# Kernel optimization log

Hardware: AMD Instinct MI355X
Metric: run time of the kernel (lower is better)

The kernel has to match this reference:

```python
import jax, jax.numpy as jnp
import numpy as np

B, N, M, D = 2, 256, 8, 256      # batch, seq, modalities, dmodel
H, DH = 8, 64                     # heads, dim_head (hardcoded defaults)
INNER = H * DH                    # 512
MULT = 4                          # FFN mult
SCALE = DH ** -0.5
EPS = 1e-5


def layer_norm(x, g, b):
    mu = jnp.mean(x, axis=-1, keepdims=True)
    var = jnp.mean((x - mu) ** 2, axis=-1, keepdims=True)
    return (x - mu) * jax.lax.rsqrt(var + EPS) * g + b


def setup_inputs() -> dict:
    key = jax.random.key(0)
    ks = jax.random.split(key, 8)
    s = 0.02
    return {
        "x": jax.random.normal(ks[0], (B, D, M, N), jnp.float32),
        "Wq": jax.random.normal(ks[1], (D, INNER), jnp.float32) * s,
        "Wkv": jax.random.normal(ks[2], (D, 2 * INNER), jnp.float32) * s,
        "Wout": jax.random.normal(ks[3], (INNER * M, D * M), jnp.float32) * s,
        "bout": jnp.zeros((D * M,), jnp.float32),
        "g1": jnp.ones((D,), jnp.float32),
        "beta1": jnp.zeros((D,), jnp.float32),
        "Wff1": jax.random.normal(ks[4], (D, 2 * D * MULT), jnp.float32) * s,
        "bff1": jnp.zeros((2 * D * MULT,), jnp.float32),
        "Wff2": jax.random.normal(ks[5], (D * MULT, D), jnp.float32) * s,
        "bff2": jnp.zeros((D,), jnp.float32),
        "g2": jnp.ones((D,), jnp.float32),
        "beta2": jnp.zeros((D,), jnp.float32),
    }


def reference(x, Wq, Wkv, Wout, bout, g1, beta1, Wff1, bff1, Wff2, bff2, g2, beta2):
    x_shape = x.shape
    xt = jnp.transpose(x, (0, 3, 2, 1))          # [B,N,M,D]
    # --- Channel_Seq_Big_Attention (self-attention, context = x) ---
    q = (xt @ Wq).reshape(B, N, M, H, DH)
    kv = xt @ Wkv
    k, v = jnp.split(kv, 2, axis=-1)
    k = k.reshape(B, N, M, H, DH)
    v = v.reshape(B, N, M, H, DH)
    # sim: [(b h), i, j, m, z] kept as [B,H,i,j,m,z]
    sim = jnp.einsum('bimhd,bjzhd->bhijmz', q, k) * SCALE
    attn = jax.nn.softmax(sim, axis=2)           # softmax over j (dim=-3 of bijmz)
    out = jnp.einsum('bhijmz,bjmhd->bizhd', attn, v)  # [B,N,M,H,DH]
    out = out.reshape(B, N, M * H * DH)          # 'b n (m h d)'
    o = (out @ Wout + bout).reshape(B, N, M, D)
    # --- residual + post-norm ---
    xt = layer_norm(xt + o, g1, beta1)
    # --- GEGLU FFN ---
    hg = xt @ Wff1 + bff1
    a, gate = jnp.split(hg, 2, axis=-1)
    ff = (a * jax.nn.gelu(gate, approximate=False)) @ Wff2 + bff2
    xt = layer_norm(xt + ff, g2, beta2)
    return xt.reshape(x_shape)                   # torch .view(x_shape)
```

## Files before the change

kernel.cpp:

```cpp
#include <hip/hip_runtime.h>
#include <math.h>

#define KS_ 0.1803368801111244f

typedef __attribute__((ext_vector_type(8))) short bf16x8;
typedef __attribute__((ext_vector_type(4))) short bf16x4;
typedef __attribute__((ext_vector_type(4))) float f32x4;

__device__ inline short f2bf(float f) {
  unsigned u = __builtin_bit_cast(unsigned, f);
  u += 0x7fff + ((u >> 16) & 1);
  return (short)(u >> 16);
}

__device__ inline void gload16(const short* g, short* l) {
  __builtin_amdgcn_global_load_lds(
      (const __attribute__((address_space(1))) void*)g,
      (__attribute__((address_space(3))) void*)l, 16, 0, 0);
}

__device__ inline void wt_tile(const float* __restrict__ W, short* __restrict__ WT,
                               int K, int N, int bx, int by, int t, float (*tile)[33]) {
  int n0 = bx * 32, k0 = by * 32;
  int tx = t & 31, ty = t >> 5;
#pragma unroll
  for (int r = 0; r < 32; r += 8)
    tile[ty + r][tx] = W[(size_t)(k0 + ty + r) * N + n0 + tx];
  __syncthreads();
#pragma unroll
  for (int r = 0; r < 32; r += 8)
    WT[(size_t)(n0 + ty + r) * K + k0 + tx] = f2bf(tile[tx][ty + r]);
}

__global__ __launch_bounds__(256) void k_prep_all(const float* __restrict__ x, float* __restrict__ xt,
                                                  short* __restrict__ xtbf,
                                                  const float* __restrict__ Wq, const float* __restrict__ Wkv,
                                                  const float* __restrict__ Wout, const float* __restrict__ Wff1,
                                                  const float* __restrict__ Wff2,
                                                  short* __restrict__ WqkvT, short* __restrict__ WoutT,
                                                  short* __restrict__ Wff1T, short* __restrict__ Wff2T) {
  __shared__ float tile[32][33];
  int bid = blockIdx.x, t = threadIdx.x;
  if (bid < 8192) {
    wt_tile(Wout, WoutT, 4096, 2048, bid & 63, bid >> 6, t, tile);
  } else if (bid < 9216) {
    int r = bid - 8192;
    int bx = r & 7, by = (r >> 3) & 7, bm = r >> 6;
    int b = bm >> 3, m = bm & 7;
    int d0 = bx * 32, n0 = by * 32;
    int tx = t & 31, ty = t >> 5;
#pragma unroll
    for (int rr = 0; rr < 32; rr += 8) {
      int d = d0 + ty + rr, n = n0 + tx;
      tile[ty + rr][tx] = x[((size_t)(b * 256 + d) * 8 + m) * 256 + n];
    }
    __syncthreads();
#pragma unroll
    for (int rr = 0; rr < 32; rr += 8) {
      int n = n0 + ty + rr, d = d0 + tx;
      float v = tile[tx][ty + rr];
      size_t idx = ((size_t)(b * 256 + n) * 8 + m) * 256 + d;
      xt[idx] = v;
      xtbf[idx] = f2bf(v);
    }
  } else if (bid < 9344) {
    int r = bid - 9216;
    wt_tile(Wq, WqkvT, 256, 512, r & 15, r >> 4, t, tile);
  } else if (bid < 9600) {
    int r = bid - 9344;
    wt_tile(Wkv, WqkvT + 131072, 256, 1024, r & 31, r >> 5, t, tile);
  } else if (bid < 10112) {
    int r = bid - 9600;
    wt_tile(Wff1, Wff1T, 256, 2048, r & 63, r >> 6, t, tile);
  } else {
    int r = bid - 10112;
    wt_tile(Wff2, Wff2T, 1024, 256, r & 7, r >> 3, t, tile);
  }
}

__global__ __launch_bounds__(256) void k_gemm_qkv(const short* __restrict__ A, const short* __restrict__ Bt,
                                                  short* __restrict__ qfrag, short* __restrict__ kfrag,
                                                  short* __restrict__ vfrag) {
  __shared__ short As[2][2048];
  __shared__ short Bs[2][2048];
  __shared__ short Cs[64 * 72];
  int t = threadIdx.x;
  int bx = blockIdx.x, by = blockIdx.y;
  int sel = bx >> 3, h = bx & 7;
  int row0 = by * 64, col0 = bx * 64;
  int b = by >> 5, n0 = (by * 8) & 255;
  int bh = b * 8 + h;
  int w = t >> 6, lane = t & 63, quad = lane >> 4, l16 = lane & 15;
  int wr = w >> 1, wc = w & 1;
  int r = t >> 2;
  int cs = ((t & 3) ^ ((r >> 1) & 3)) * 8;
  const short* Ag = A + (size_t)(row0 + r) * 256 + cs;
  const short* Bg = Bt + (size_t)(col0 + r) * 256 + cs;
  int sw = (l16 >> 1) & 3;
  int chk = (quad ^ sw) * 8;
  int aoff[2], boff[2];
#pragma unroll
  for (int rf = 0; rf < 2; rf++) {
    aoff[rf] = (wr * 32 + rf * 16 + l16) * 32 + chk;
    boff[rf] = (wc * 32 + rf * 16 + l16) * 32 + chk;
  }
  f32x4 acc[2][2] = {{{0,0,0,0},{0,0,0,0}},{{0,0,0,0},{0,0,0,0}}};
  gload16(Ag, &As[0][w * 512]);
  gload16(Bg, &Bs[0][w * 512]);
  __syncthreads();
  int buf = 0;
  for (int k0 = 0; k0 < 256; k0 += 32) {
    int nb = buf ^ 1;
    if (k0 + 32 < 256) {
      gload16(Ag + k0 + 32, &As[nb][w * 512]);
      gload16(Bg + k0 + 32, &Bs[nb][w * 512]);
    }
    bf16x8 af[2], bf[2];
#pragma unroll
    for (int rf = 0; rf < 2; rf++) af[rf] = *(const bf16x8*)&As[buf][aoff[rf]];
#pragma unroll
    for (int cf = 0; cf < 2; cf++) bf[cf] = *(const bf16x8*)&Bs[buf][boff[cf]];
#pragma unroll
    for (int rf = 0; rf < 2; rf++)
#pragma unroll
      for (int cf = 0; cf < 2; cf++)
        acc[rf][cf] = __builtin_amdgcn_mfma_f32_16x16x32_bf16(af[rf], bf[cf], acc[rf][cf], 0, 0, 0);
    __syncthreads();
    buf = nb;
  }
  if (sel < 2) {
#pragma unroll
    for (int rf = 0; rf < 2; rf++)
#pragma unroll
      for (int cf = 0; cf < 2; cf++) {
        int col = wc * 32 + cf * 16 + l16;
#pragma unroll
        for (int rr = 0; rr < 4; rr++)
          Cs[(wr * 32 + rf * 16 + quad * 4 + rr) * 72 + col] = f2bf(acc[rf][cf][rr]);
      }
  } else {
#pragma unroll
    for (int rf = 0; rf < 2; rf++)
#pragma unroll
      for (int cf = 0; cf < 2; cf++) {
        int col = wc * 32 + cf * 16 + l16;
        bf16x4 pk;
#pragma unroll
        for (int rr = 0; rr < 4; rr++) pk[rr] = f2bf(acc[rf][cf][rr]);
        *(bf16x4*)&Cs[col * 72 + wr * 32 + rf * 16 + quad * 4] = pk;
      }
  }
  __syncthreads();
  if (sel < 2) {
    short* dst = sel ? kfrag : qfrag;
    int it = n0 >> 4, l16b = n0 & 8;
#pragma unroll
    for (int cidx = 0; cidx < 2; cidx++) {
      int chunk = t + cidx * 256;
      int m = chunk >> 6, ks2 = (chunk >> 5) & 1, q2 = (chunk >> 3) & 3, n = chunk & 7;
      bf16x8 val = *(const bf16x8*)&Cs[(n * 8 + m) * 72 + ks2 * 32 + q2 * 8];
      size_t off = ((size_t)(bh * 128 + m * 16 + it) * 2 + ks2) * 512 + (q2 * 16 + l16b + n) * 8;
      *(bf16x8*)(dst + off) = val;
    }
  } else {
    int jc = n0 >> 5, jf = (n0 >> 4) & 1, qbase = (n0 & 8) >> 2;
#pragma unroll
    for (int cidx = 0; cidx < 2; cidx++) {
      int chunk = t + cidx * 256;
      int qd = chunk >> 8, m0 = (chunk >> 6) & 3, dtt = (chunk >> 4) & 3, l16c = chunk & 15;
      int d = dtt * 16 + l16c;
      unsigned u[4];
#pragma unroll
      for (int e3 = 0; e3 < 4; e3++)
        u[e3] = *(const unsigned*)&Cs[d * 72 + qd * 32 + e3 * 8 + 2 * m0];
      uint4 pv;
      pv.x = __builtin_amdgcn_perm(u[1], u[0], 0x05040100u);
      pv.y = __builtin_amdgcn_perm(u[3], u[2], 0x05040100u);
      pv.z = __builtin_amdgcn_perm(u[1], u[0], 0x07060302u);
      pv.w = __builtin_amdgcn_perm(u[3], u[2], 0x07060302u);
      int quad2 = qbase + qd;
      size_t cid = (((size_t)(bh * 8 + jc) * 4 + m0) * 4 + dtt) * 2 + jf;
      *(bf16x8*)(vfrag + cid * 512 + (quad2 * 16 + l16c) * 8) = __builtin_bit_cast(bf16x8, pv);
    }
  }
}

__global__ __launch_bounds__(256) void k_gemm128(const short* __restrict__ A, const short* __restrict__ Bt,
                                                 const float* __restrict__ bias, float* __restrict__ C,
                                                 int M, int N, int K, int Ks) {
  __shared__ short As[2][4096];
  __shared__ short Bs[2][4096];
  int t = threadIdx.x;
  int row0 = blockIdx.y * 128, col0 = blockIdx.x * 128;
  int kp = blockIdx.z;
  int kbeg = kp * Ks, kend = kbeg + Ks;
  int w = t >> 6, lane = t & 63, quad = lane >> 4, l16 = lane & 15;
  int wr = w >> 1, wc = w & 1;
  int rs = t >> 2;
  int cs = ((t & 3) ^ ((rs >> 1) & 3)) * 8;
  const short* Ag = A + (size_t)(row0 + rs) * K + cs;
  const short* Bg = Bt + (size_t)(col0 + rs) * K + cs;
  size_t rskip = (size_t)64 * K;
  int chk = (quad ^ ((l16 >> 1) & 3)) * 8;
  int aoff[4], boff[4];
#pragma unroll
  for (int f = 0; f < 4; f++) {
    aoff[f] = (wr * 64 + f * 16 + l16) * 32 + chk;
    boff[f] = (wc * 64 + f * 16 + l16) * 32 + chk;
  }
  f32x4 acc[4][4];
#pragma unroll
  for (int i = 0; i < 4; i++)
#pragma unroll
    for (int j = 0; j < 4; j++) acc[i][j] = (f32x4){0, 0, 0, 0};
  int ld0 = w * 512;
  gload16(Ag + kbeg, &As[0][ld0]);
  gload16(Ag + rskip + kbeg, &As[0][2048 + ld0]);
  gload16(Bg + kbeg, &Bs[0][ld0]);
  gload16(Bg + rskip + kbeg, &Bs[0][2048 + ld0]);
  __syncthreads();
  int buf = 0;
  for (int k0 = kbeg; k0 < kend; k0 += 32) {
    int nb = buf ^ 1;
    if (k0 + 32 < kend) {
      gload16(Ag + k0 + 32, &As[nb][ld0]);
      gload16(Ag + rskip + k0 + 32, &As[nb][2048 + ld0]);
      gload16(Bg + k0 + 32, &Bs[nb][ld0]);
      gload16(Bg + rskip + k0 + 32, &Bs[nb][2048 + ld0]);
    }
    bf16x8 af[4], bf[4];
#pragma unroll
    for (int f = 0; f < 4; f++) af[f] = *(const bf16x8*)&As[buf][aoff[f]];
#pragma unroll
    for (int f = 0; f < 4; f++) bf[f] = *(const bf16x8*)&Bs[buf][boff[f]];
#pragma unroll
    for (int i = 0; i < 4; i++)
#pragma unroll
      for (int j = 0; j < 4; j++)
        acc[i][j] = __builtin_amdgcn_mfma_f32_16x16x32_bf16(af[i], bf[j], acc[i][j], 0, 0, 0);
    __syncthreads();
    buf = nb;
  }
  float* Cp = C + (size_t)kp * M * N;
  bool dob = (bias && kp == 0);
#pragma unroll
  for (int i = 0; i < 4; i++)
#pragma unroll
    for (int j = 0; j < 4; j++) {
      int col = col0 + wc * 64 + j * 16 + l16;
      float vb = dob ? bias[col] : 0.0f;
#pragma unroll
      for (int rr = 0; rr < 4; rr++) {
        int row = row0 + wr * 64 + i * 16 + quad * 4 + rr;
        Cp[(size_t)row * N + col] = acc[i][j][rr] + vb;
      }
    }
}

__global__ __launch_bounds__(256) void k_gemm_bf(const short* __restrict__ A, const short* __restrict__ Bt,
                                                 const float* __restrict__ bias, float* __restrict__ C,
                                                 int M, int N, int K, int Ks) {
  __shared__ short As[2][2048];
  __shared__ short Bs[2][2048];
  int t = threadIdx.x;
  int row0 = blockIdx.y * 64, col0 = blockIdx.x * 64;
  int kp = blockIdx.z;
  int kbeg = kp * Ks, kend = kbeg + Ks;
  int w = t >> 6, lane = t & 63, quad = lane >> 4, l16 = lane & 15;
  int wr = w >> 1, wc = w & 1;
  int r = t >> 2;
  int cs = ((t & 3) ^ ((r >> 1) & 3)) * 8;
  const short* Ag = A + (size_t)(row0 + r) * K + cs;
  const short* Bg = Bt + (size_t)(col0 + r) * K + cs;
  int sw = (l16 >> 1) & 3;
  int chk = (quad ^ sw) * 8;
  int aoff[2], boff[2];
#pragma unroll
  for (int rf = 0; rf < 2; rf++) {
    aoff[rf] = (wr * 32 + rf * 16 + l16) * 32 + chk;
    boff[rf] = (wc * 32 + rf * 16 + l16) * 32 + chk;
  }
  f32x4 acc[2][2] = {{{0,0,0,0},{0,0,0,0}},{{0,0,0,0},{0,0,0,0}}};
  gload16(Ag + kbeg, &As[0][w * 512]);
  gload16(Bg + kbeg, &Bs[0][w * 512]);
  __syncthreads();
  int buf = 0;
  for (int k0 = kbeg; k0 < kend; k0 += 32) {
    int nb = buf ^ 1;
    if (k0 + 32 < kend) {
      gload16(Ag + k0 + 32, &As[nb][w * 512]);
      gload16(Bg + k0 + 32, &Bs[nb][w * 512]);
    }
    bf16x8 af[2], bf[2];
#pragma unroll
    for (int rf = 0; rf < 2; rf++) af[rf] = *(const bf16x8*)&As[buf][aoff[rf]];
#pragma unroll
    for (int cf = 0; cf < 2; cf++) bf[cf] = *(const bf16x8*)&Bs[buf][boff[cf]];
#pragma unroll
    for (int rf = 0; rf < 2; rf++)
#pragma unroll
      for (int cf = 0; cf < 2; cf++)
        acc[rf][cf] = __builtin_amdgcn_mfma_f32_16x16x32_bf16(af[rf], bf[cf], acc[rf][cf], 0, 0, 0);
    __syncthreads();
    buf = nb;
  }
  float* Cp = C + (size_t)kp * M * N;
#pragma unroll
  for (int rf = 0; rf < 2; rf++)
#pragma unroll
    for (int cf = 0; cf < 2; cf++) {
      int col = col0 + wc * 32 + cf * 16 + l16;
      float vb = (bias && kp == 0) ? bias[col] : 0.0f;
#pragma unroll
      for (int rr = 0; rr < 4; rr++) {
        int row = row0 + wr * 32 + rf * 16 + quad * 4 + rr;
        Cp[(size_t)row * N + col] = acc[rf][cf][rr] + vb;
      }
    }
}

__global__ __launch_bounds__(256) void k_ff1g128(const short* __restrict__ A, const short* __restrict__ Bt,
                                                 const float* __restrict__ bias, short* __restrict__ gg) {
  __shared__ short As[2][4096];
  __shared__ short Ba[2][2048];
  __shared__ short Bg[2][2048];
  int t = threadIdx.x;
  int colA0 = blockIdx.x * 64, row0 = blockIdx.y * 128;
  int w = t >> 6, lane = t & 63, quad = lane >> 4, l16 = lane & 15;
  int wr = w >> 1, wc = w & 1;
  int rs = t >> 2;
  int cs = ((t & 3) ^ ((rs >> 1) & 3)) * 8;
  const short* Ag  = A + (size_t)(row0 + rs) * 256 + cs;
  const short* BaG = Bt + (size_t)(colA0 + rs) * 256 + cs;
  const short* BgG = Bt + (size_t)(1024 + colA0 + rs) * 256 + cs;
  int chk = (quad ^ ((l16 >> 1) & 3)) * 8;
  int aoff[4], boff[2];
#pragma unroll
  for (int f = 0; f < 4; f++) aoff[f] = (wr * 64 + f * 16 + l16) * 32 + chk;
#pragma unroll
  for (int f = 0; f < 2; f++) boff[f] = (wc * 32 + f * 16 + l16) * 32 + chk;
  f32x4 za = {0, 0, 0, 0};
  f32x4 acc_a[4][2] = {{za, za}, {za, za}, {za, za}, {za, za}};
  f32x4 acc_g[4][2] = {{za, za}, {za, za}, {za, za}, {za, za}};
  int ld0 = w * 512;
  gload16(Ag, &As[0][ld0]);
  gload16(Ag + (size_t)64 * 256, &As[0][2048 + ld0]);
  gload16(BaG, &Ba[0][ld0]);
  gload16(BgG, &Bg[0][ld0]);
  __syncthreads();
  int buf = 0;
  for (int k0 = 0; k0 < 256; k0 += 32) {
    int nb = buf ^ 1;
    if (k0 + 32 < 256) {
      gload16(Ag + k0 + 32, &As[nb][ld0]);
      gload16(Ag + (size_t)64 * 256 + k0 + 32, &As[nb][2048 + ld0]);
      gload16(BaG + k0 + 32, &Ba[nb][ld0]);
      gload16(BgG + k0 + 32, &Bg[nb][ld0]);
    }
    bf16x8 af[4], ba[2], bg[2];
#pragma unroll
    for (int f = 0; f < 4; f++) af[f] = *(const bf16x8*)&As[buf][aoff[f]];
#pragma unroll
    for (int f = 0; f < 2; f++) {
      ba[f] = *(const bf16x8*)&Ba[buf][boff[f]];
      bg[f] = *(const bf16x8*)&Bg[buf][boff[f]];
    }
#pragma unroll
    for (int i = 0; i < 4; i++)
#pragma unroll
      for (int j = 0; j < 2; j++) {
        acc_a[i][j] = __builtin_amdgcn_mfma_f32_16x16x32_bf16(af[i], ba[j], acc_a[i][j], 0, 0, 0);
        acc_g[i][j] = __builtin_amdgcn_mfma_f32_16x16x32_bf16(af[i], bg[j], acc_g[i][j], 0, 0, 0);
      }
    __syncthreads();
    buf = nb;
  }
#pragma unroll
  for (int i = 0; i < 4; i++)
#pragma unroll
    for (int j = 0; j < 2; j++) {
      int col = colA0 + wc * 32 + j * 16 + l16;
      float ba_ = bias[col], bg_ = bias[1024 + col];
#pragma unroll
      for (int rr = 0; rr < 4; rr++) {
        int row = row0 + wr * 64 + i * 16 + quad * 4 + rr;
        float a = acc_a[i][j][rr] + ba_;
        float g = acc_g[i][j][rr] + bg_;
        float ge = 0.5f * g * (1.0f + erff(g * 0.70710678118654752f));
        gg[(size_t)row * 1024 + col] = f2bf(a * ge);
      }
    }
}

__global__ __launch_bounds__(256) void k_attn_den5(const short* __restrict__ qfrag, const short* __restrict__ kfrag,
                                                   float* __restrict__ rdg) {
  int ct2 = blockIdx.x, mp = blockIdx.y, bh = blockIdx.z;
  int t = threadIdx.x;
  int w = t >> 6, lane = t & 63;
  int rt0 = ct2 * 8 + w * 2;
  bf16x8 bfr[2][2];
#pragma unroll
  for (int cf = 0; cf < 2; cf++)
#pragma unroll
    for (int ks = 0; ks < 2; ks++)
      bfr[cf][ks] = *(const bf16x8*)(kfrag + ((size_t)((bh * 128 + rt0 + cf) * 2 + ks)) * 512 + lane * 8);
  for (int mi = 0; mi < 2; mi++) {
    int m = mp * 2 + mi;
    float fa0 = 0.0f, fa1 = 0.0f;
#pragma unroll 4
    for (int it2 = 0; it2 < 16; it2++) {
      const short* ap = qfrag + ((size_t)((bh * 128 + m * 16 + it2) * 2)) * 512 + lane * 8;
      bf16x8 a0 = *(const bf16x8*)ap;
      bf16x8 a1 = *(const bf16x8*)(ap + 512);
      f32x4 c0 = {0, 0, 0, 0}, c1 = {0, 0, 0, 0};
      c0 = __builtin_amdgcn_mfma_f32_16x16x32_bf16(a0, bfr[0][0], c0, 0, 0, 0);
      c0 = __builtin_amdgcn_mfma_f32_16x16x32_bf16(a1, bfr[0][1], c0, 0, 0, 0);
      c1 = __builtin_amdgcn_mfma_f32_16x16x32_bf16(a0, bfr[1][0], c1, 0, 0, 0);
      c1 = __builtin_amdgcn_mfma_f32_16x16x32_bf16(a1, bfr[1][1], c1, 0, 0, 0);
#pragma unroll
      for (int rr = 0; rr < 4; rr++) {
        fa0 += __builtin_amdgcn_exp2f(c0[rr] * KS_);
        fa1 += __builtin_amdgcn_exp2f(c1[rr] * KS_);
      }
    }
    fa0 += __shfl_xor(fa0, 16); fa0 += __shfl_xor(fa0, 32);
    fa1 += __shfl_xor(fa1, 16); fa1 += __shfl_xor(fa1, 32);
    if (lane < 16) {
      rdg[(size_t)(bh * 8 + m) * 2048 + rt0 * 16 + lane] = -__builtin_amdgcn_logf(fa0);
      rdg[(size_t)(bh * 8 + m) * 2048 + (rt0 + 1) * 16 + lane] = -__builtin_amdgcn_logf(fa1);
    }
  }
}

__global__ __launch_bounds__(256) void k_attn_out6(const short* __restrict__ qfrag, const short* __restrict__ kfrag,
                                                   const short* __restrict__ vfrag, const float* __restrict__ rdg,
                                                   short* __restrict__ ao) {
  __shared__ float red[4 * 64 * 17];
  int z = blockIdx.x, itp = blockIdx.y, bh = blockIdx.z;
  int b = bh >> 3, h = bh & 7;
  int t = threadIdx.x, w = t >> 6, lane = t & 63, quad = lane >> 4, l16 = lane & 15;
  const float* rb = rdg + (size_t)bh * 16384;
  f32x4 z4 = {0, 0, 0, 0};
  bf16x8 qf[2][2][2];
#pragma unroll
  for (int iti = 0; iti < 2; iti++)
#pragma unroll
    for (int mm = 0; mm < 2; mm++)
#pragma unroll
      for (int ks = 0; ks < 2; ks++)
        qf[iti][mm][ks] = *(const bf16x8*)(qfrag +
            ((size_t)((bh * 128 + (2 * w + mm) * 16 + itp * 2 + iti) * 2 + ks)) * 512 + lane * 8);
  f32x4 acc[2][4];
#pragma unroll
  for (int iti = 0; iti < 2; iti++)
#pragma unroll
    for (int dt = 0; dt < 4; dt++) acc[iti][dt] = z4;
  bf16x8 vf[4][2], kf[2][2];
  float4 nv0[2], nv1[2];
#pragma unroll
  for (int dt = 0; dt < 4; dt++)
#pragma unroll
    for (int jf = 0; jf < 2; jf++)
      vf[dt][jf] = *(const bf16x8*)(vfrag + ((((size_t)(bh * 8 + 0) * 4 + w) * 4 + dt) * 2 + jf) * 512 + lane * 8);
#pragma unroll
  for (int jf = 0; jf < 2; jf++) {
    const short* kp = kfrag + ((size_t)((bh * 128 + z * 16 + 0 * 2 + jf) * 2)) * 512 + lane * 8;
    kf[jf][0] = *(const bf16x8*)kp;
    kf[jf][1] = *(const bf16x8*)(kp + 512);
    nv0[jf] = *(const float4*)(rb + (size_t)(2 * w) * 2048 + z * 256 + 0 * 32 + jf * 16 + quad * 4);
    nv1[jf] = *(const float4*)(rb + (size_t)(2 * w + 1) * 2048 + z * 256 + 0 * 32 + jf * 16 + quad * 4);
  }
  for (int jc = 0; jc < 8; jc++) {
    bf16x8 vfn[4][2], kfn[2][2];
    float4 nv0n[2], nv1n[2];
    if (jc < 7) {
      int jn = jc + 1;
#pragma unroll
      for (int dt = 0; dt < 4; dt++)
#pragma unroll
        for (int jf = 0; jf < 2; jf++)
          vfn[dt][jf] = *(const bf16x8*)(vfrag + ((((size_t)(bh * 8 + jn) * 4 + w) * 4 + dt) * 2 + jf) * 512 + lane * 8);
#pragma unroll
      for (int jf = 0; jf < 2; jf++) {
        const short* kp = kfrag + ((size_t)((bh * 128 + z * 16 + jn * 2 + jf) * 2)) * 512 + lane * 8;
        kfn[jf][0] = *(const bf16x8*)kp;
        kfn[jf][1] = *(const bf16x8*)(kp + 512);
        nv0n[jf] = *(const float4*)(rb + (size_t)(2 * w) * 2048 + z * 256 + jn * 32 + jf * 16 + quad * 4);
        nv1n[jf] = *(const float4*)(rb + (size_t)(2 * w + 1) * 2048 + z * 256 + jn * 32 + jf * 16 + quad * 4);
      }
    }
    float n0[2][4] = {{nv0[0].x, nv0[0].y, nv0[0].z, nv0[0].w}, {nv0[1].x, nv0[1].y, nv0[1].z, nv0[1].w}};
    float n1[2][4] = {{nv1[0].x, nv1[0].y, nv1[0].z, nv1[0].w}, {nv1[1].x, nv1[1].y, nv1[1].z, nv1[1].w}};
#pragma unroll
    for (int iti = 0; iti < 2; iti++) {
      f32x4 c[2][2] = {{z4, z4}, {z4, z4}};
#pragma unroll
      for (int jf = 0; jf < 2; jf++)
#pragma unroll
        for (int mm = 0; mm < 2; mm++) {
          c[jf][mm] = __builtin_amdgcn_mfma_f32_16x16x32_bf16(kf[jf][0], qf[iti][mm][0], c[jf][mm], 0, 0, 0);
          c[jf][mm] = __builtin_amdgcn_mfma_f32_16x16x32_bf16(kf[jf][1], qf[iti][mm][1], c[jf][mm], 0, 0, 0);
        }
      bf16x8 pf[2];
#pragma unroll
      for (int jf = 0; jf < 2; jf++) {
        unsigned u[8];
#pragma unroll
        for (int e = 0; e < 4; e++) {
          u[e]     = __builtin_bit_cast(unsigned, __builtin_amdgcn_exp2f(fmaf(c[jf][0][e], KS_, n0[jf][e]))) + 0x8000u;
          u[e + 4] = __builtin_bit_cast(unsigned, __builtin_amdgcn_exp2f(fmaf(c[jf][1][e], KS_, n1[jf][e]))) + 0x8000u;
        }
        uint4 pv;
        pv.x = __builtin_amdgcn_perm(u[1], u[0], 0x07060302u);
        pv.y = __builtin_amdgcn_perm(u[3], u[2], 0x07060302u);
        pv.z = __builtin_amdgcn_perm(u[5], u[4], 0x07060302u);
        pv.w = __builtin_amdgcn_perm(u[7], u[6], 0x07060302u);
        pf[jf] = __builtin_bit_cast(bf16x8, pv);
      }
#pragma unroll
      for (int dt = 0; dt < 4; dt++)
#pragma unroll
        for (int jf = 0; jf < 2; jf++)
          acc[iti][dt] = __builtin_amdgcn_mfma_f32_16x16x32_bf16(vf[dt][jf], pf[jf], acc[iti][dt], 0, 0, 0);
    }
    if (jc < 7) {
#pragma unroll
      for (int dt = 0; dt < 4; dt++)
#pragma unroll
        for (int jf = 0; jf < 2; jf++) vf[dt][jf] = vfn[dt][jf];
#pragma unroll
      for (int jf = 0; jf < 2; jf++) {
        kf[jf][0] = kfn[jf][0]; kf[jf][1] = kfn[jf][1];
        nv0[jf] = nv0n[jf]; nv1[jf] = nv1n[jf];
      }
    }
  }
  for (int iti = 0; iti < 2; iti++) {
#pragma unroll
    for (int dt = 0; dt < 4; dt++)
#pragma unroll
      for (int rr = 0; rr < 4; rr++)
        red[w * 1088 + (dt * 16 + quad * 4 + rr) * 17 + l16] = acc[iti][dt][rr];
    __syncthreads();
    {
      int i = t >> 4, dg = t & 15;
      float s[4] = {0, 0, 0, 0};
#pragma unroll
      for (int w2 = 0; w2 < 4; w2++)
#pragma unroll
        for (int r2 = 0; r2 < 4; r2++)
          s[r2] += red[w2 * 1088 + (dg * 4 + r2) * 17 + i];
      bf16x4 ov;
#pragma unroll
      for (int r2 = 0; r2 < 4; r2++) ov[r2] = f2bf(s[r2]);
      *(bf16x4*)(ao + (size_t)((b * 256 + itp * 32 + iti * 16 + i) * 8 + z) * 512 + h * 64 + dg * 4) = ov;
    }
    __syncthreads();
  }
}

__global__ __launch_bounds__(256) void k_ln(const float* __restrict__ X, const float* __restrict__ P, int np,
                                            const float* __restrict__ g, const float* __restrict__ be,
                                            float* __restrict__ Y, short* __restrict__ Ybf) {
  __shared__ float sm[8];
  int row = blockIdx.x, t = threadIdx.x;
  int lane = t & 63, w = t >> 6;
  size_t base = (size_t)row * 256;
  float v = X[base + t];
  for (int p = 0; p < np; p++) v += P[(size_t)p * 1048576 + base + t];
  float s = v;
  s += __shfl_xor(s, 1); s += __shfl_xor(s, 2); s += __shfl_xor(s, 4);
  s += __shfl_xor(s, 8); s += __shfl_xor(s, 16); s += __shfl_xor(s, 32);
  if (lane == 0) sm[w] = s;
  __syncthreads();
  float mu = (sm[0] + sm[1] + sm[2] + sm[3]) * (1.0f / 256.0f);
  float dv = v - mu;
  float s2 = dv * dv;
  s2 += __shfl_xor(s2, 1); s2 += __shfl_xor(s2, 2); s2 += __shfl_xor(s2, 4);
  s2 += __shfl_xor(s2, 8); s2 += __shfl_xor(s2, 16); s2 += __shfl_xor(s2, 32);
  if (lane == 0) sm[4 + w] = s2;
  __syncthreads();
  float var = (sm[4] + sm[5] + sm[6] + sm[7]) * (1.0f / 256.0f);
  float rs = rsqrtf(var + 1e-5f);
  float res = dv * rs * g[t] + be[t];
  Y[base + t] = res;
  if (Ybf) Ybf[base + t] = f2bf(res);
}

extern "C" void kernel_launch(void* const* d_in, const int* in_sizes, int n_in,
                              void* d_out, int out_size, void* d_ws, size_t ws_size,
                              hipStream_t stream) {
  const float* x    = (const float*)d_in[0];
  const float* Wq   = (const float*)d_in[1];
  const float* Wkv  = (const float*)d_in[2];
  const float* Wout = (const float*)d_in[3];
  const float* bout = (const float*)d_in[4];
  const float* g1   = (const float*)d_in[5];
  const float* be1  = (const float*)d_in[6];
  const float* Wff1 = (const float*)d_in[7];
  const float* bff1 = (const float*)d_in[8];
  const float* Wff2 = (const float*)d_in[9];
  const float* bff2 = (const float*)d_in[10];
  const float* g2   = (const float*)d_in[11];
  const float* be2  = (const float*)d_in[12];
  float* out = (float*)d_out;
  float* w = (float*)d_ws;

  float* xt   = w;
  float* part = w + 1048576;
  float* y    = w + 9437184;
  float* rdg  = w + 11534336;
  short* sb     = (short*)(w + 11796480);
  short* qfrag  = sb;
  short* kfrag  = sb + 2097152;
  short* vfrag  = sb + 4194304;
  short* xt_bf  = sb + 6291456;
  short* ao_bf  = sb + 7340032;
  short* y_bf   = sb + 9437184;
  short* gg_bf  = sb + 10485760;
  short* WqkvT  = sb + 14680064;
  short* WoutT  = sb + 15073280;
  short* Wff1T  = sb + 23461888;
  short* Wff2T  = sb + 23986176;

  k_prep_all<<<10368, 256, 0, stream>>>(x, xt, xt_bf, Wq, Wkv, Wout, Wff1, Wff2,
                                        WqkvT, WoutT, Wff1T, Wff2T);
  k_gemm_qkv<<<dim3(24, 64), 256, 0, stream>>>(xt_bf, WqkvT, qfrag, kfrag, vfrag);
  k_attn_den5<<<dim3(16, 4, 16), 256, 0, stream>>>(qfrag, kfrag, rdg);
  k_attn_out6<<<dim3(8, 8, 16), 256, 0, stream>>>(qfrag, kfrag, vfrag, rdg, ao_bf);
  k_gemm128<<<dim3(16, 4, 8), 256, 0, stream>>>(ao_bf, WoutT, bout, part, 512, 2048, 4096, 512);
  k_ln<<<4096, 256, 0, stream>>>(xt, part, 8, g1, be1, y, y_bf);
  k_ff1g128<<<dim3(16, 32), 256, 0, stream>>>(y_bf, Wff1T, bff1, gg_bf);
  k_gemm_bf<<<dim3(4, 64, 4), 256, 0, stream>>>(gg_bf, Wff2T, bff2, part, 4096, 256, 1024, 256);
  k_ln<<<4096, 256, 0, stream>>>(y, part, 4, g2, be2, out, nullptr);
}
```

Measured before the change: 220.8 us.

## Fuse output projection, layernorms and FFN into one cooperative persistent kernel

Replaces five separate launches (out-projection GEMM, LN1, GEGLU FF1, FF2 GEMM, LN2) with a single cooperative kernel of 256 blocks of 512 threads. Each block runs two 256-thread sub-tiles and the stages are separated by grid-wide syncs. FF2 now uses 2 K-splits instead of 4, and each LN sub-tile handles 8 rows. The aim is to remove per-launch overhead and tail gaps between stages. The cost is grid.sync barriers, fixed occupancy of one block per CU, and less parallelism in the LN and FF2 stages.

```diff
diff --git a/kernel.cpp b/kernel.cpp
--- a/kernel.cpp
+++ b/kernel.cpp
@@ -1,5 +1,8 @@
 #include <hip/hip_runtime.h>
+#include <hip/hip_cooperative_groups.h>
 #include <math.h>
+
+namespace cg = cooperative_groups;
 
 #define KS_ 0.1803368801111244f
 
@@ -185,213 +188,6 @@
   }
 }
 
-__global__ __launch_bounds__(256) void k_gemm128(const short* __restrict__ A, const short* __restrict__ Bt,
-                                                 const float* __restrict__ bias, float* __restrict__ C,
-                                                 int M, int N, int K, int Ks) {
-  __shared__ short As[2][4096];
-  __shared__ short Bs[2][4096];
-  int t = threadIdx.x;
-  int row0 = blockIdx.y * 128, col0 = blockIdx.x * 128;
-  int kp = blockIdx.z;
-  int kbeg = kp * Ks, kend = kbeg + Ks;
-  int w = t >> 6, lane = t & 63, quad = lane >> 4, l16 = lane & 15;
-  int wr = w >> 1, wc = w & 1;
-  int rs = t >> 2;
-  int cs = ((t & 3) ^ ((rs >> 1) & 3)) * 8;
-  const short* Ag = A + (size_t)(row0 + rs) * K + cs;
-  const short* Bg = Bt + (size_t)(col0 + rs) * K + cs;
-  size_t rskip = (size_t)64 * K;
-  int chk = (quad ^ ((l16 >> 1) & 3)) * 8;
-  int aoff[4], boff[4];
-#pragma unroll
-  for (int f = 0; f < 4; f++) {
-    aoff[f] = (wr * 64 + f * 16 + l16) * 32 + chk;
-    boff[f] = (wc * 64 + f * 16 + l16) * 32 + chk;
-  }
-  f32x4 acc[4][4];
-#pragma unroll
-  for (int i = 0; i < 4; i++)
-#pragma unroll
-    for (int j = 0; j < 4; j++) acc[i][j] = (f32x4){0, 0, 0, 0};
-  int ld0 = w * 512;
-  gload16(Ag + kbeg, &As[0][ld0]);
-  gload16(Ag + rskip + kbeg, &As[0][2048 + ld0]);
-  gload16(Bg + kbeg, &Bs[0][ld0]);
-  gload16(Bg + rskip + kbeg, &Bs[0][2048 + ld0]);
-  __syncthreads();
-  int buf = 0;
-  for (int k0 = kbeg; k0 < kend; k0 += 32) {
-    int nb = buf ^ 1;
-    if (k0 + 32 < kend) {
-      gload16(Ag + k0 + 32, &As[nb][ld0]);
-      gload16(Ag + rskip + k0 + 32, &As[nb][2048 + ld0]);
-      gload16(Bg + k0 + 32, &Bs[nb][ld0]);
-      gload16(Bg + rskip + k0 + 32, &Bs[nb][2048 + ld0]);
-    }
-    bf16x8 af[4], bf[4];
-#pragma unroll
-    for (int f = 0; f < 4; f++) af[f] = *(const bf16x8*)&As[buf][aoff[f]];
-#pragma unroll
-    for (int f = 0; f < 4; f++) bf[f] = *(const bf16x8*)&Bs[buf][boff[f]];
-#pragma unroll
-    for (int i = 0; i < 4; i++)
-#pragma unroll
-      for (int j = 0; j < 4; j++)
-        acc[i][j] = __builtin_amdgcn_mfma_f32_16x16x32_bf16(af[i], bf[j], acc[i][j], 0, 0, 0);
-    __syncthreads();
-    buf = nb;
-  }
-  float* Cp = C + (size_t)kp * M * N;
-  bool dob = (bias && kp == 0);
-#pragma unroll
-  for (int i = 0; i < 4; i++)
-#pragma unroll
-    for (int j = 0; j < 4; j++) {
-      int col = col0 + wc * 64 + j * 16 + l16;
-      float vb = dob ? bias[col] : 0.0f;
-#pragma unroll
-      for (int rr = 0; rr < 4; rr++) {
-        int row = row0 + wr * 64 + i * 16 + quad * 4 + rr;
-        Cp[(size_t)row * N + col] = acc[i][j][rr] + vb;
-      }
-    }
-}
-
-__global__ __launch_bounds__(256) void k_gemm_bf(const short* __restrict__ A, const short* __restrict__ Bt,
-                                                 const float* __restrict__ bias, float* __restrict__ C,
-                                                 int M, int N, int K, int Ks) {
-  __shared__ short As[2][2048];
-  __shared__ short Bs[2][2048];
-  int t = threadIdx.x;
-  int row0 = blockIdx.y * 64, col0 = blockIdx.x * 64;
-  int kp = blockIdx.z;
-  int kbeg = kp * Ks, kend = kbeg + Ks;
-  int w = t >> 6, lane = t & 63, quad = lane >> 4, l16 = lane & 15;
-  int wr = w >> 1, wc = w & 1;
-  int r = t >> 2;
-  int cs = ((t & 3) ^ ((r >> 1) & 3)) * 8;
-  const short* Ag = A + (size_t)(row0 + r) * K + cs;
-  const short* Bg = Bt + (size_t)(col0 + r) * K + cs;
-  int sw = (l16 >> 1) & 3;
-  int chk = (quad ^ sw) * 8;
-  int aoff[2], boff[2];
-#pragma unroll
-  for (int rf = 0; rf < 2; rf++) {
-    aoff[rf] = (wr * 32 + rf * 16 + l16) * 32 + chk;
-    boff[rf] = (wc * 32 + rf * 16 + l16) * 32 + chk;
-  }
-  f32x4 acc[2][2] = {{{0,0,0,0},{0,0,0,0}},{{0,0,0,0},{0,0,0,0}}};
-  gload16(Ag + kbeg, &As[0][w * 512]);
-  gload16(Bg + kbeg, &Bs[0][w * 512]);
-  __syncthreads();
-  int buf = 0;
-  for (int k0 = kbeg; k0 < kend; k0 += 32) {
-    int nb = buf ^ 1;
-    if (k0 + 32 < kend) {
-      gload16(Ag + k0 + 32, &As[nb][w * 512]);
-      gload16(Bg + k0 + 32, &Bs[nb][w * 512]);
-    }
-    bf16x8 af[2], bf[2];
-#pragma unroll
-    for (int rf = 0; rf < 2; rf++) af[rf] = *(const bf16x8*)&As[buf][aoff[rf]];
-#pragma unroll
-    for (int cf = 0; cf < 2; cf++) bf[cf] = *(const bf16x8*)&Bs[buf][boff[cf]];
-#pragma unroll
-    for (int rf = 0; rf < 2; rf++)
-#pragma unroll
-      for (int cf = 0; cf < 2; cf++)
-        acc[rf][cf] = __builtin_amdgcn_mfma_f32_16x16x32_bf16(af[rf], bf[cf], acc[rf][cf], 0, 0, 0);
-    __syncthreads();
-    buf = nb;
-  }
-  float* Cp = C + (size_t)kp * M * N;
-#pragma unroll
-  for (int rf = 0; rf < 2; rf++)
-#pragma unroll
-    for (int cf = 0; cf < 2; cf++) {
-      int col = col0 + wc * 32 + cf * 16 + l16;
-      float vb = (bias && kp == 0) ? bias[col] : 0.0f;
-#pragma unroll
-      for (int rr = 0; rr < 4; rr++) {
-        int row = row0 + wr * 32 + rf * 16 + quad * 4 + rr;
-        Cp[(size_t)row * N + col] = acc[rf][cf][rr] + vb;
-      }
-    }
-}
-
-__global__ __launch_bounds__(256) void k_ff1g128(const short* __restrict__ A, const short* __restrict__ Bt,
-                                                 const float* __restrict__ bias, short* __restrict__ gg) {
-  __shared__ short As[2][4096];
-  __shared__ short Ba[2][2048];
-  __shared__ short Bg[2][2048];
-  int t = threadIdx.x;
-  int colA0 = blockIdx.x * 64, row0 = blockIdx.y * 128;
-  int w = t >> 6, lane = t & 63, quad = lane >> 4, l16 = lane & 15;
-  int wr = w >> 1, wc = w & 1;
-  int rs = t >> 2;
-  int cs = ((t & 3) ^ ((rs >> 1) & 3)) * 8;
-  const short* Ag  = A + (size_t)(row0 + rs) * 256 + cs;
-  const short* BaG = Bt + (size_t)(colA0 + rs) * 256 + cs;
-  const short* BgG = Bt + (size_t)(1024 + colA0 + rs) * 256 + cs;
-  int chk = (quad ^ ((l16 >> 1) & 3)) * 8;
-  int aoff[4], boff[2];
-#pragma unroll
-  for (int f = 0; f < 4; f++) aoff[f] = (wr * 64 + f * 16 + l16) * 32 + chk;
-#pragma unroll
-  for (int f = 0; f < 2; f++) boff[f] = (wc * 32 + f * 16 + l16) * 32 + chk;
-  f32x4 za = {0, 0, 0, 0};
-  f32x4 acc_a[4][2] = {{za, za}, {za, za}, {za, za}, {za, za}};
-  f32x4 acc_g[4][2] = {{za, za}, {za, za}, {za, za}, {za, za}};
-  int ld0 = w * 512;
-  gload16(Ag, &As[0][ld0]);
-  gload16(Ag + (size_t)64 * 256, &As[0][2048 + ld0]);
-  gload16(BaG, &Ba[0][ld0]);
-  gload16(BgG, &Bg[0][ld0]);
-  __syncthreads();
-  int buf = 0;
-  for (int k0 = 0; k0 < 256; k0 += 32) {
-    int nb = buf ^ 1;
-    if (k0 + 32 < 256) {
-      gload16(Ag + k0 + 32, &As[nb][ld0]);
-      gload16(Ag + (size_t)64 * 256 + k0 + 32, &As[nb][2048 + ld0]);
-      gload16(BaG + k0 + 32, &Ba[nb][ld0]);
-      gload16(BgG + k0 + 32, &Bg[nb][ld0]);
-    }
-    bf16x8 af[4], ba[2], bg[2];
-#pragma unroll
-    for (int f = 0; f < 4; f++) af[f] = *(const bf16x8*)&As[buf][aoff[f]];
-#pragma unroll
-    for (int f = 0; f < 2; f++) {
-      ba[f] = *(const bf16x8*)&Ba[buf][boff[f]];
-      bg[f] = *(const bf16x8*)&Bg[buf][boff[f]];
-    }
-#pragma unroll
-    for (int i = 0; i < 4; i++)
-#pragma unroll
-      for (int j = 0; j < 2; j++) {
-        acc_a[i][j] = __builtin_amdgcn_mfma_f32_16x16x32_bf16(af[i], ba[j], acc_a[i][j], 0, 0, 0);
-        acc_g[i][j] = __builtin_amdgcn_mfma_f32_16x16x32_bf16(af[i], bg[j], acc_g[i][j], 0, 0, 0);
-      }
-    __syncthreads();
-    buf = nb;
-  }
-#pragma unroll
-  for (int i = 0; i < 4; i++)
-#pragma unroll
-    for (int j = 0; j < 2; j++) {
-      int col = colA0 + wc * 32 + j * 16 + l16;
-      float ba_ = bias[col], bg_ = bias[1024 + col];
-#pragma unroll
-      for (int rr = 0; rr < 4; rr++) {
-        int row = row0 + wr * 64 + i * 16 + quad * 4 + rr;
-        float a = acc_a[i][j][rr] + ba_;
-        float g = acc_g[i][j][rr] + bg_;
-        float ge = 0.5f * g * (1.0f + erff(g * 0.70710678118654752f));
-        gg[(size_t)row * 1024 + col] = f2bf(a * ge);
-      }
-    }
-}
-
 __global__ __launch_bounds__(256) void k_attn_den5(const short* __restrict__ qfrag, const short* __restrict__ kfrag,
                                                    float* __restrict__ rdg) {
   int ct2 = blockIdx.x, mp = blockIdx.y, bh = blockIdx.z;
@@ -559,32 +355,271 @@
   }
 }
 
-__global__ __launch_bounds__(256) void k_ln(const float* __restrict__ X, const float* __restrict__ P, int np,
-                                            const float* __restrict__ g, const float* __restrict__ be,
-                                            float* __restrict__ Y, short* __restrict__ Ybf) {
-  __shared__ float sm[8];
-  int row = blockIdx.x, t = threadIdx.x;
-  int lane = t & 63, w = t >> 6;
-  size_t base = (size_t)row * 256;
-  float v = X[base + t];
-  for (int p = 0; p < np; p++) v += P[(size_t)p * 1048576 + base + t];
-  float s = v;
-  s += __shfl_xor(s, 1); s += __shfl_xor(s, 2); s += __shfl_xor(s, 4);
-  s += __shfl_xor(s, 8); s += __shfl_xor(s, 16); s += __shfl_xor(s, 32);
-  if (lane == 0) sm[w] = s;
+
+__device__ __forceinline__ void gemm128_body(const short* __restrict__ A, const short* __restrict__ Bt,
+                                             const float* __restrict__ bias, float* __restrict__ C,
+                                             int N, int K, int kbeg, int kend, int row0, int col0,
+                                             int tl, short* L, bool dob) {
+  short* As = L;
+  short* Bs = L + 8192;
+  int w = tl >> 6, lane = tl & 63, quad = lane >> 4, l16 = lane & 15;
+  int wr = w >> 1, wc = w & 1;
+  int rs = tl >> 2;
+  int cs = ((tl & 3) ^ ((rs >> 1) & 3)) * 8;
+  const short* Ag = A + (size_t)(row0 + rs) * K + cs;
+  const short* Bg = Bt + (size_t)(col0 + rs) * K + cs;
+  size_t rskip = (size_t)64 * K;
+  int chk = (quad ^ ((l16 >> 1) & 3)) * 8;
+  int aoff[4], boff[4];
+#pragma unroll
+  for (int f = 0; f < 4; f++) {
+    aoff[f] = (wr * 64 + f * 16 + l16) * 32 + chk;
+    boff[f] = (wc * 64 + f * 16 + l16) * 32 + chk;
+  }
+  f32x4 acc[4][4];
+#pragma unroll
+  for (int i = 0; i < 4; i++)
+#pragma unroll
+    for (int j = 0; j < 4; j++) acc[i][j] = (f32x4){0, 0, 0, 0};
+  int ld0 = w * 512;
+  gload16(Ag + kbeg, &As[ld0]);
+  gload16(Ag + rskip + kbeg, &As[2048 + ld0]);
+  gload16(Bg + kbeg, &Bs[ld0]);
+  gload16(Bg + rskip + kbeg, &Bs[2048 + ld0]);
   __syncthreads();
-  float mu = (sm[0] + sm[1] + sm[2] + sm[3]) * (1.0f / 256.0f);
-  float dv = v - mu;
-  float s2 = dv * dv;
-  s2 += __shfl_xor(s2, 1); s2 += __shfl_xor(s2, 2); s2 += __shfl_xor(s2, 4);
-  s2 += __shfl_xor(s2, 8); s2 += __shfl_xor(s2, 16); s2 += __shfl_xor(s2, 32);
-  if (lane == 0) sm[4 + w] = s2;
+  int buf = 0;
+  for (int k0 = kbeg; k0 < kend; k0 += 32) {
+    int nb = buf ^ 1;
+    if (k0 + 32 < kend) {
+      gload16(Ag + k0 + 32, &As[nb * 4096 + ld0]);
+      gload16(Ag + rskip + k0 + 32, &As[nb * 4096 + 2048 + ld0]);
+      gload16(Bg + k0 + 32, &Bs[nb * 4096 + ld0]);
+      gload16(Bg + rskip + k0 + 32, &Bs[nb * 4096 + 2048 + ld0]);
+    }
+    bf16x8 af[4], bf[4];
+#pragma unroll
+    for (int f = 0; f < 4; f++) af[f] = *(const bf16x8*)&As[buf * 4096 + aoff[f]];
+#pragma unroll
+    for (int f = 0; f < 4; f++) bf[f] = *(const bf16x8*)&Bs[buf * 4096 + boff[f]];
+#pragma unroll
+    for (int i = 0; i < 4; i++)
+#pragma unroll
+      for (int j = 0; j < 4; j++)
+        acc[i][j] = __builtin_amdgcn_mfma_f32_16x16x32_bf16(af[i], bf[j], acc[i][j], 0, 0, 0);
+    __syncthreads();
+    buf = nb;
+  }
+#pragma unroll
+  for (int i = 0; i < 4; i++)
+#pragma unroll
+    for (int j = 0; j < 4; j++) {
+      int col = col0 + wc * 64 + j * 16 + l16;
+      float vb = dob ? bias[col] : 0.0f;
+#pragma unroll
+      for (int rr = 0; rr < 4; rr++) {
+        int row = row0 + wr * 64 + i * 16 + quad * 4 + rr;
+        C[(size_t)row * N + col] = acc[i][j][rr] + vb;
+      }
+    }
+}
+
+__device__ __forceinline__ void gemm64_body(const short* __restrict__ A, const short* __restrict__ Bt,
+                                            const float* __restrict__ bias, float* __restrict__ C,
+                                            int N, int K, int kbeg, int kend, int row0, int col0,
+                                            int tl, short* L, bool dob) {
+  short* As = L;
+  short* Bs = L + 4096;
+  int w = tl >> 6, lane = tl & 63, quad = lane >> 4, l16 = lane & 15;
+  int wr = w >> 1, wc = w & 1;
+  int rs = tl >> 2;
+  int cs = ((tl & 3) ^ ((rs >> 1) & 3)) * 8;
+  const short* Ag = A + (size_t)(row0 + rs) * K + cs;
+  const short* Bg = Bt + (size_t)(col0 + rs) * K + cs;
+  int chk = (quad ^ ((l16 >> 1) & 3)) * 8;
+  int aoff[2], boff[2];
+#pragma unroll
+  for (int rf = 0; rf < 2; rf++) {
+    aoff[rf] = (wr * 32 + rf * 16 + l16) * 32 + chk;
+    boff[rf] = (wc * 32 + rf * 16 + l16) * 32 + chk;
+  }
+  f32x4 acc[2][2] = {{{0,0,0,0},{0,0,0,0}},{{0,0,0,0},{0,0,0,0}}};
+  int ld0 = w * 512;
+  gload16(Ag + kbeg, &As[ld0]);
+  gload16(Bg + kbeg, &Bs[ld0]);
   __syncthreads();
-  float var = (sm[4] + sm[5] + sm[6] + sm[7]) * (1.0f / 256.0f);
-  float rs = rsqrtf(var + 1e-5f);
-  float res = dv * rs * g[t] + be[t];
-  Y[base + t] = res;
-  if (Ybf) Ybf[base + t] = f2bf(res);
+  int buf = 0;
+  for (int k0 = kbeg; k0 < kend; k0 += 32) {
+    int nb = buf ^ 1;
+    if (k0 + 32 < kend) {
+      gload16(Ag + k0 + 32, &As[nb * 2048 + ld0]);
+      gload16(Bg + k0 + 32, &Bs[nb * 2048 + ld0]);
+    }
+    bf16x8 af[2], bf[2];
+#pragma unroll
+    for (int rf = 0; rf < 2; rf++) af[rf] = *(const bf16x8*)&As[buf * 2048 + aoff[rf]];
+#pragma unroll
+    for (int cf = 0; cf < 2; cf++) bf[cf] = *(const bf16x8*)&Bs[buf * 2048 + boff[cf]];
+#pragma unroll
+    for (int rf = 0; rf < 2; rf++)
+#pragma unroll
+      for (int cf = 0; cf < 2; cf++)
+        acc[rf][cf] = __builtin_amdgcn_mfma_f32_16x16x32_bf16(af[rf], bf[cf], acc[rf][cf], 0, 0, 0);
+    __syncthreads();
+    buf = nb;
+  }
+#pragma unroll
+  for (int rf = 0; rf < 2; rf++)
+#pragma unroll
+    for (int cf = 0; cf < 2; cf++) {
+      int col = col0 + wc * 32 + cf * 16 + l16;
+      float vb = dob ? bias[col] : 0.0f;
+#pragma unroll
+      for (int rr = 0; rr < 4; rr++) {
+        int row = row0 + wr * 32 + rf * 16 + quad * 4 + rr;
+        C[(size_t)row * N + col] = acc[rf][cf][rr] + vb;
+      }
+    }
+}
+
+__device__ __forceinline__ void ff1_body(const short* __restrict__ A, const short* __restrict__ Bt,
+                                         const float* __restrict__ bias, short* __restrict__ gg,
+                                         int row0, int colA0, int tl, short* L) {
+  short* As = L;
+  short* Ba = L + 8192;
+  short* Bg = L + 12288;
+  int w = tl >> 6, lane = tl & 63, quad = lane >> 4, l16 = lane & 15;
+  int wr = w >> 1, wc = w & 1;
+  int rs = tl >> 2;
+  int cs = ((tl & 3) ^ ((rs >> 1) & 3)) * 8;
+  const short* Ag  = A + (size_t)(row0 + rs) * 256 + cs;
+  const short* BaG = Bt + (size_t)(colA0 + rs) * 256 + cs;
+  const short* BgG = Bt + (size_t)(1024 + colA0 + rs) * 256 + cs;
+  int chk = (quad ^ ((l16 >> 1) & 3)) * 8;
+  int aoff[4], boff[2];
+#pragma unroll
+  for (int f = 0; f < 4; f++) aoff[f] = (wr * 64 + f * 16 + l16) * 32 + chk;
+#pragma unroll
+  for (int f = 0; f < 2; f++) boff[f] = (wc * 32 + f * 16 + l16) * 32 + chk;
+  f32x4 za = {0, 0, 0, 0};
+  f32x4 acc_a[4][2] = {{za, za}, {za, za}, {za, za}, {za, za}};
+  f32x4 acc_g[4][2] = {{za, za}, {za, za}, {za, za}, {za, za}};
+  int ld0 = w * 512;
+  gload16(Ag, &As[ld0]);
+  gload16(Ag + (size_t)64 * 256, &As[2048 + ld0]);
+  gload16(BaG, &Ba[ld0]);
+  gload16(BgG, &Bg[ld0]);
+  __syncthreads();
+  int buf = 0;
+  for (int k0 = 0; k0 < 256; k0 += 32) {
+    int nb = buf ^ 1;
+    if (k0 + 32 < 256) {
+      gload16(Ag + k0 + 32, &As[nb * 4096 + ld0]);
+      gload16(Ag + (size_t)64 * 256 + k0 + 32, &As[nb * 4096 + 2048 + ld0]);
+      gload16(BaG + k0 + 32, &Ba[nb * 2048 + ld0]);
+      gload16(BgG + k0 + 32, &Bg[nb * 2048 + ld0]);
+    }
+    bf16x8 af[4], ba[2], bg[2];
+#pragma unroll
+    for (int f = 0; f < 4; f++) af[f] = *(const bf16x8*)&As[buf * 4096 + aoff[f]];
+#pragma unroll
+    for (int f = 0; f < 2; f++) {
+      ba[f] = *(const bf16x8*)&Ba[buf * 2048 + boff[f]];
+      bg[f] = *(const bf16x8*)&Bg[buf * 2048 + boff[f]];
+    }
+#pragma unroll
+    for (int i = 0; i < 4; i++)
+#pragma unroll
+      for (int j = 0; j < 2; j++) {
+        acc_a[i][j] = __builtin_amdgcn_mfma_f32_16x16x32_bf16(af[i], ba[j], acc_a[i][j], 0, 0, 0);
+        acc_g[i][j] = __builtin_amdgcn_mfma_f32_16x16x32_bf16(af[i], bg[j], acc_g[i][j], 0, 0, 0);
+      }
+    __syncthreads();
+    buf = nb;
+  }
+#pragma unroll
+  for (int i = 0; i < 4; i++)
+#pragma unroll
+    for (int j = 0; j < 2; j++) {
+      int col = colA0 + wc * 32 + j * 16 + l16;
+      float ba_ = bias[col], bg_ = bias[1024 + col];
+#pragma unroll
+      for (int rr = 0; rr < 4; rr++) {
+        int row = row0 + wr * 64 + i * 16 + quad * 4 + rr;
+        float a = acc_a[i][j][rr] + ba_;
+        float g = acc_g[i][j][rr] + bg_;
+        float ge = 0.5f * g * (1.0f + erff(g * 0.70710678118654752f));
+        gg[(size_t)row * 1024 + col] = f2bf(a * ge);
+      }
+    }
+}
+
+__device__ __forceinline__ void ln_body(const float* __restrict__ X, const float* __restrict__ P, int np,
+                                        const float* __restrict__ g, const float* __restrict__ be,
+                                        float* __restrict__ Y, short* __restrict__ Ybf,
+                                        int s, int tl, float* smf) {
+  int lane = tl & 63, w = tl >> 6;
+  for (int rr = 0; rr < 8; rr++) {
+    int row = s * 8 + rr;
+    size_t base = (size_t)row * 256;
+    float v = X[base + tl];
+    for (int p = 0; p < np; p++) v += P[(size_t)p * 1048576 + base + tl];
+    float sum = v;
+    sum += __shfl_xor(sum, 1); sum += __shfl_xor(sum, 2); sum += __shfl_xor(sum, 4);
+    sum += __shfl_xor(sum, 8); sum += __shfl_xor(sum, 16); sum += __shfl_xor(sum, 32);
+    if (lane == 0) smf[w] = sum;
+    __syncthreads();
+    float mu = (smf[0] + smf[1] + smf[2] + smf[3]) * (1.0f / 256.0f);
+    float dv = v - mu;
+    float s2 = dv * dv;
+    s2 += __shfl_xor(s2, 1); s2 += __shfl_xor(s2, 2); s2 += __shfl_xor(s2, 4);
+    s2 += __shfl_xor(s2, 8); s2 += __shfl_xor(s2, 16); s2 += __shfl_xor(s2, 32);
+    if (lane == 0) smf[4 + w] = s2;
+    __syncthreads();
+    float var = (smf[4] + smf[5] + smf[6] + smf[7]) * (1.0f / 256.0f);
+    float rs_ = rsqrtf(var + 1e-5f);
+    float res = dv * rs_ * g[tl] + be[tl];
+    Y[base + tl] = res;
+    if (Ybf) Ybf[base + tl] = f2bf(res);
+    __syncthreads();
+  }
+}
+
+__global__ __launch_bounds__(512) void k_tail(const short* __restrict__ ao, const short* __restrict__ WoutT,
+                                              const float* __restrict__ bout,
+                                              const float* __restrict__ xt, const float* __restrict__ g1,
+                                              const float* __restrict__ be1,
+                                              const short* __restrict__ Wff1T, const float* __restrict__ bff1,
+                                              const short* __restrict__ Wff2T, const float* __restrict__ bff2,
+                                              const float* __restrict__ g2, const float* __restrict__ be2,
+                                              float* __restrict__ part, float* __restrict__ y,
+                                              short* __restrict__ ybf, short* __restrict__ gg,
+                                              float* __restrict__ out) {
+  __shared__ short lds[2][16384];
+  cg::grid_group grid = cg::this_grid();
+  int t = threadIdx.x;
+  int sub = t >> 8, tl = t & 255;
+  int s = blockIdx.x * 2 + sub;
+  short* L = lds[sub];
+  {
+    int kp = s & 7, colT = (s >> 3) & 15, rowT = s >> 7;
+    gemm128_body(ao, WoutT, bout, part + (size_t)kp * 1048576, 2048, 4096,
+                 kp * 512, kp * 512 + 512, rowT * 128, colT * 128, tl, L, kp == 0);
+  }
+  grid.sync();
+  ln_body(xt, part, 8, g1, be1, y, ybf, s, tl, (float*)L);
+  grid.sync();
+  {
+    int colT = s & 15, rowT = s >> 4;
+    ff1_body(ybf, Wff1T, bff1, gg, rowT * 128, colT * 64, tl, L);
+  }
+  grid.sync();
+  {
+    int kp = s & 1, colT = (s >> 1) & 3, rowT = s >> 3;
+    gemm64_body(gg, Wff2T, bff2, part + (size_t)kp * 1048576, 256, 1024,
+                kp * 512, kp * 512 + 512, rowT * 64, colT * 64, tl, L, kp == 0);
+  }
+  grid.sync();
+  ln_body(y, part, 2, g2, be2, out, nullptr, s, tl, (float*)L);
 }
 
 extern "C" void kernel_launch(void* const* d_in, const int* in_sizes, int n_in,
@@ -628,9 +663,14 @@
   k_gemm_qkv<<<dim3(24, 64), 256, 0, stream>>>(xt_bf, WqkvT, qfrag, kfrag, vfrag);
   k_attn_den5<<<dim3(16, 4, 16), 256, 0, stream>>>(qfrag, kfrag, rdg);
   k_attn_out6<<<dim3(8, 8, 16), 256, 0, stream>>>(qfrag, kfrag, vfrag, rdg, ao_bf);
-  k_gemm128<<<dim3(16, 4, 8), 256, 0, stream>>>(ao_bf, WoutT, bout, part, 512, 2048, 4096, 512);
-  k_ln<<<4096, 256, 0, stream>>>(xt, part, 8, g1, be1, y, y_bf);
-  k_ff1g128<<<dim3(16, 32), 256, 0, stream>>>(y_bf, Wff1T, bff1, gg_bf);
-  k_gemm_bf<<<dim3(4, 64, 4), 256, 0, stream>>>(gg_bf, Wff2T, bff2, part, 4096, 256, 1024, 256);
-  k_ln<<<4096, 256, 0, stream>>>(y, part, 4, g2, be2, out, nullptr);
-}
+  {
+    void* args[] = {(void*)&ao_bf, (void*)&WoutT, (void*)&bout,
+                    (void*)&xt, (void*)&g1, (void*)&be1,
+                    (void*)&Wff1T, (void*)&bff1,
+                    (void*)&Wff2T, (void*)&bff2,
+                    (void*)&g2, (void*)&be2,
+                    (void*)&part, (void*)&y, (void*)&y_bf, (void*)&gg_bf, (void*)&out};
+    hipLaunchCooperativeKernel(reinterpret_cast<void*>(k_tail), dim3(256), dim3(512),
+                               args, 0, stream);
+  }
+}
```

Measured after the change: 375.9 us. 1.7x slower.
